# Performance work log

Hardware: AMD Instinct MI355X
Metric: run time of the kernel (lower is better)

## Reference

```python
import jax, jax.numpy as jnp
import numpy as np

N = 50000      # nodes
E = 800000     # unique directed edges (avg degree 16)
F = 64         # input_dim
D = 64         # output_dim (== F -> residual is identity)
ALPHA = 0.5
LCS_THR = 0.5  # enable_lcs_masking=True, lcs_threshold=0.5


def setup_inputs() -> dict:
    key = jax.random.key(0)
    ks = jax.random.split(key, 16)
    x = jax.random.normal(ks[0], (N, F), jnp.float32)
    src = jax.random.randint(ks[1], (E,), 0, N, jnp.int32)
    dst = jax.random.randint(ks[2], (E,), 0, N, jnp.int32)
    # integer-valued multiplicities in {1,2,3,4} (recurring-transaction counts)
    counts = jnp.floor(jax.random.uniform(ks[3], (E,), jnp.float32) * 4.0) + 1.0
    def lin(k, fan_in, shape):
        return jax.random.normal(k, shape, jnp.float32) / np.float32(np.sqrt(fan_in))
    return dict(
        x=x, counts=counts,
        W_s2d=lin(ks[4], F, (F, D)), b_s2d=jnp.zeros((D,), jnp.float32),
        W_d2s=lin(ks[5], F, (F, D)), b_d2s=jnp.zeros((D,), jnp.float32),
        W_l1=lin(ks[6], 2 * F, (2 * F, F)), b_l1=jnp.zeros((F,), jnp.float32),
        W_l2=lin(ks[7], F, (F, 1)), b_l2=jnp.zeros((1,), jnp.float32),
        W_g1=lin(ks[8], 2 * D, (2 * D, D)), b_g1=jnp.zeros((D,), jnp.float32),
        W_g2=lin(ks[9], D, (D, 1)), b_g2=jnp.zeros((1,), jnp.float32),
        src=src, dst=dst,
    )


def reference(x, counts, W_s2d, b_s2d, W_d2s, b_d2s,
              W_l1, b_l1, W_l2, b_l2, W_g1, b_g1, W_g2, b_g2,
              src, dst):
    # in/out degrees from full (unmasked) multiplicities, clamped at 1
    in_deg = jnp.maximum(jax.ops.segment_sum(counts, dst, num_segments=N), 1.0)
    out_deg = jnp.maximum(jax.ops.segment_sum(counts, src, num_segments=N), 1.0)

    # LCS per unique edge: sigmoid(MLP([x_src, x_dst])), detached in torch
    lcs_in = jnp.concatenate([x[src], x[dst]], axis=-1)          # [E, 2F]
    lcs = jax.nn.sigmoid(
        jax.nn.relu(lcs_in @ W_l1 + b_l1) @ W_l2 + b_l2)[:, 0]   # [E]
    lcs = jax.lax.stop_gradient(lcs)
    keep = (lcs >= LCS_THR).astype(x.dtype)                      # LCS masking

    # symmetric-normalized edge weights with multiplicity counts
    w = counts * keep * jax.lax.rsqrt(out_deg[src] * in_deg[dst])  # [E]

    # direction-aware message passing (redundancy-eliminated, per unique edge)
    h_s2d = x @ W_s2d + b_s2d                                    # [N, D]
    h_d2s = x @ W_d2s + b_d2s                                    # [N, D]
    m_in = jax.ops.segment_sum(w[:, None] * h_s2d[src], dst, num_segments=N)
    m_out = jax.ops.segment_sum(w[:, None] * h_d2s[dst], src, num_segments=N)

    # node-wise gating over inbound vs outbound flows
    gate = jax.nn.sigmoid(
        jax.nn.relu(jnp.concatenate([m_in, m_out], axis=-1) @ W_g1 + b_g1)
        @ W_g2 + b_g2)                                           # [N, 1]

    # gated alpha-blend + identity residual (input_dim == output_dim)
    out = ALPHA * gate * m_in + (1.0 - ALPHA) * (1.0 - gate) * m_out + x
    return out
```

## Files before the change

### kernel.cpp

```cpp
#include <hip/hip_runtime.h>
#include <math.h>


typedef unsigned long long u64;

__device__ __forceinline__ float bflo(unsigned u) { return __uint_as_float(u << 16); }
__device__ __forceinline__ float bfhi(unsigned u) { return __uint_as_float(u & 0xffff0000u); }
__device__ __forceinline__ unsigned rne16(float f) {
    unsigned u = __float_as_uint(f);
    return (u + 0x7fffu + ((u >> 16) & 1u)) >> 16;
}

__global__ void zero_kernel(int* __restrict__ p, int n) {
    int i = blockIdx.x * blockDim.x + threadIdx.x;
    int stride = gridDim.x * blockDim.x;
    for (int j = i; j < n; j += stride) p[j] = 0;
}

__global__ void finalize_deg_kernel(const u64* __restrict__ hd_pack,
                                    const u64* __restrict__ hs_pack,
                                    float* __restrict__ isq_in, float* __restrict__ isq_out, int N) {
    int i = blockIdx.x * blockDim.x + threadIdx.x;
    if (i < N) {
        isq_in[i]  = 1.f / sqrtf(fmaxf((float)(unsigned)hd_pack[i], 1.f));
        isq_out[i] = 1.f / sqrtf(fmaxf((float)(unsigned)hs_pack[i], 1.f));
    }
}

__global__ __launch_bounds__(256) void proj_kernel(
    const float* __restrict__ x,
    const float* __restrict__ Wl1,  const float* __restrict__ bl1,
    const float* __restrict__ Ws2d, const float* __restrict__ bs2d,
    const float* __restrict__ Wd2s, const float* __restrict__ bd2s,
    float* __restrict__ A, float* __restrict__ B,
    unsigned* __restrict__ Ah, unsigned* __restrict__ Bh,
    unsigned* __restrict__ HSh, unsigned* __restrict__ HDh, int N)
{
    __shared__ float xs[64][64];
    const int tid = threadIdx.x;
    const int n0  = blockIdx.x * 64;
    const int wv  = tid >> 6;
    const int cc  = tid & 63;

    const float* Wbase; const float* bias; float* obase; unsigned* obh;
    switch (wv) {
        case 0:  Wbase = Wl1;           bias = bl1;     obase = A;       obh = Ah;  break;
        case 1:  Wbase = Wl1 + 64 * 64; bias = nullptr; obase = B;       obh = Bh;  break;
        case 2:  Wbase = Ws2d;          bias = bs2d;    obase = nullptr; obh = HSh; break;
        default: Wbase = Wd2s;          bias = bd2s;    obase = nullptr; obh = HDh; break;
    }

    float wr[64];
#pragma unroll
    for (int k = 0; k < 64; ++k) wr[k] = Wbase[k * 64 + cc];
    const float bv = bias ? bias[cc] : 0.f;

#pragma unroll
    for (int j = 0; j < 4; ++j) {
        int f4  = tid + j * 256;
        int row = f4 >> 4;
        int c4  = f4 & 15;
        int gn  = n0 + row;
        float4 v = (gn < N) ? ((const float4*)x)[(long)gn * 16 + c4]
                            : make_float4(0.f, 0.f, 0.f, 0.f);
        ((float4*)&xs[row][0])[c4] = v;
    }
    __syncthreads();

    const int nmax = (N - n0 < 64) ? (N - n0) : 64;
    for (int n = 0; n < nmax; ++n) {
        float acc = bv;
#pragma unroll
        for (int k = 0; k < 64; k += 4) {
            float4 xv = *((const float4*)&xs[n][k]);
            acc += xv.x * wr[k] + xv.y * wr[k + 1] + xv.z * wr[k + 2] + xv.w * wr[k + 3];
        }
        if (obase) obase[(long)(n0 + n) * 64 + cc] = acc;
        const float part = __shfl_xor(acc, 1);
        if ((cc & 1) == 0)
            obh[(long)(n0 + n) * 32 + (cc >> 1)] = (rne16(part) << 16) | rne16(acc);
    }
}

#define LCS_MARGIN 0.04f
__global__ __launch_bounds__(256) void edge_w_kernel(
    const int* __restrict__ src, const int* __restrict__ dst,
    const float* __restrict__ counts,
    const float* __restrict__ A, const float* __restrict__ B,
    const unsigned* __restrict__ Ah, const unsigned* __restrict__ Bh,
    const float* __restrict__ Wl2, const float* __restrict__ bl2,
    unsigned char* __restrict__ keepc,
    u64* __restrict__ hd_pack, u64* __restrict__ hs_pack, int E)
{
    const int tid = threadIdx.x;
    const int e   = blockIdx.x * 16 + (tid >> 4);
    const int c   = tid & 15;
    if (e >= E) return;

    const int s = src[e];
    const int d = dst[e];
    const uint2 ua = *((const uint2*)(Ah + (long)s * 32 + c * 2));
    const uint2 ub = *((const uint2*)(Bh + (long)d * 32 + c * 2));
    const float4 wl = *((const float4*)(Wl2 + c * 4));

    float p = fmaxf(bflo(ua.x) + bflo(ub.x), 0.f) * wl.x
            + fmaxf(bfhi(ua.x) + bfhi(ub.x), 0.f) * wl.y
            + fmaxf(bflo(ua.y) + bflo(ub.y), 0.f) * wl.z
            + fmaxf(bfhi(ua.y) + bfhi(ub.y), 0.f) * wl.w;
    p += __shfl_xor(p, 1); p += __shfl_xor(p, 2);
    p += __shfl_xor(p, 4); p += __shfl_xor(p, 8);

    float z = p + bl2[0];
    if (fabsf(z) < LCS_MARGIN) {
        const float4 a = *((const float4*)(A + (long)s * 64 + c * 4));
        const float4 b = *((const float4*)(B + (long)d * 64 + c * 4));
        float q = fmaxf(a.x + b.x, 0.f) * wl.x + fmaxf(a.y + b.y, 0.f) * wl.y
                + fmaxf(a.z + b.z, 0.f) * wl.z + fmaxf(a.w + b.w, 0.f) * wl.w;
        q += __shfl_xor(q, 1); q += __shfl_xor(q, 2);
        q += __shfl_xor(q, 4); q += __shfl_xor(q, 8);
        z = q + bl2[0];
    }

    if (c == 0) {
        const u64 keep = (z >= 0.f) ? 1ull : 0ull;
        keepc[e] = (unsigned char)keep;
        const u64 ic = (u64)(unsigned)__float2int_rn(counts[e]);
        atomicAdd(hd_pack + d, (keep << 32) | ic);
        atomicAdd(hs_pack + s, (keep << 32) | ic);
    }
}

__global__ __launch_bounds__(256) void scan_reduce_kernel(
    const u64* __restrict__ hd_pack, const u64* __restrict__ hs_pack,
    int* __restrict__ bsum, int N, int NCH)
{
    __shared__ int sh[256];
    const int a = blockIdx.x / NCH;
    const int c = blockIdx.x - a * NCH;
    const u64* h = a ? hs_pack : hd_pack;
    const int idx = c * 256 + threadIdx.x;
    sh[threadIdx.x] = (idx < N) ? (int)(h[idx] >> 32) : 0;
    __syncthreads();
#pragma unroll
    for (int off = 128; off > 0; off >>= 1) {
        if (threadIdx.x < off) sh[threadIdx.x] += sh[threadIdx.x + off];
        __syncthreads();
    }
    if (threadIdx.x == 0) bsum[a * NCH + c] = sh[0];
}

__global__ __launch_bounds__(256) void scan_offsets_kernel(
    const int* __restrict__ bsum, int* __restrict__ boff, int NCH)
{
    __shared__ int sh[2][256];
    for (int a = 0; a < 2; ++a) {
        int v = (threadIdx.x < NCH) ? bsum[a * NCH + threadIdx.x] : 0;
        sh[0][threadIdx.x] = v;
        __syncthreads();
        int pb = 0;
        for (int off = 1; off < 256; off <<= 1) {
            int nv = sh[pb][threadIdx.x] + ((threadIdx.x >= off) ? sh[pb][threadIdx.x - off] : 0);
            sh[pb ^ 1][threadIdx.x] = nv;
            pb ^= 1;
            __syncthreads();
        }
        if (threadIdx.x < NCH) boff[a * NCH + threadIdx.x] = sh[pb][threadIdx.x] - v;
        __syncthreads();
    }
}

__global__ __launch_bounds__(256) void scan_write_kernel(
    const u64* __restrict__ hd_pack, const u64* __restrict__ hs_pack,
    const int* __restrict__ boff,
    int* __restrict__ rp_dst, int* __restrict__ cur_dst,
    int* __restrict__ rp_src, int* __restrict__ cur_src, int N, int NCH)
{
    __shared__ int sh[2][256];
    const int a = blockIdx.x / NCH;
    const int c = blockIdx.x - a * NCH;
    const u64* h = a ? hs_pack : hd_pack;
    int* rp  = a ? rp_src  : rp_dst;
    int* cur = a ? cur_src : cur_dst;
    const int idx = c * 256 + threadIdx.x;
    const int v = (idx < N) ? (int)(h[idx] >> 32) : 0;
    sh[0][threadIdx.x] = v;
    __syncthreads();
    int pb = 0;
    for (int off = 1; off < 256; off <<= 1) {
        int nv = sh[pb][threadIdx.x] + ((threadIdx.x >= off) ? sh[pb][threadIdx.x - off] : 0);
        sh[pb ^ 1][threadIdx.x] = nv;
        pb ^= 1;
        __syncthreads();
    }
    if (idx < N) {
        const int ex = sh[pb][threadIdx.x] - v + boff[a * NCH + c];
        rp[idx]  = ex;
        cur[idx] = ex;
    }
}

__global__ void scatter_kernel(const int* __restrict__ src, const int* __restrict__ dst,
                               const float* __restrict__ counts,
                               const unsigned char* __restrict__ keepc,
                               const float* __restrict__ isqo, const float* __restrict__ isqi,
                               int* __restrict__ cur_dst, int* __restrict__ cur_src,
                               unsigned* __restrict__ rec_dst, unsigned* __restrict__ rec_src, int E)
{
    int e = blockIdx.x * blockDim.x + threadIdx.x;
    if (e >= E) return;
    if (keepc[e]) {
        const int s = src[e];
        const int d = dst[e];
        const unsigned wb = rne16(counts[e] * isqo[s] * isqi[d]);
        int p = atomicAdd(cur_dst + d, 1);
        rec_dst[p] = ((unsigned)s << 16) | wb;
        int q = atomicAdd(cur_src + s, 1);
        rec_src[q] = ((unsigned)d << 16) | wb;
    }
}

__global__ __launch_bounds__(256) void gather_gate_kernel(
    const int* __restrict__ rp_dst, const int* __restrict__ cur_dst, const unsigned* __restrict__ rec_dst,
    const int* __restrict__ rp_src, const int* __restrict__ cur_src, const unsigned* __restrict__ rec_src,
    const unsigned* __restrict__ HSh, const unsigned* __restrict__ HDh,
    const float* __restrict__ x,
    const float* __restrict__ Wg1, const float* __restrict__ bg1,
    const float* __restrict__ Wg2, const float* __restrict__ bg2,
    float* __restrict__ out, int N)
{
    __shared__ float mbuf[4][128];
    const int tid  = threadIdx.x;
    const int wv   = tid >> 6;
    const int lane = tid & 63;
    const int g    = lane >> 3;
    const int c    = lane & 7;
    const int n    = blockIdx.x * 4 + wv;
    if (n >= N) return;

    float mi[8], mo[8];
#pragma unroll
    for (int j = 0; j < 8; ++j) { mi[j] = 0.f; mo[j] = 0.f; }

    {
        const int end = cur_dst[n];
        int i = rp_dst[n] + g;
        for (; i + 8 < end; i += 16) {
            const unsigned ra = rec_dst[i];
            const unsigned rb = rec_dst[i + 8];
            const float wa = bflo(ra), wb = bflo(rb);
            const uint4 ua = *((const uint4*)(HSh + (long)(ra >> 16) * 32 + c * 4));
            const uint4 ub = *((const uint4*)(HSh + (long)(rb >> 16) * 32 + c * 4));
            mi[0] += wa * bflo(ua.x) + wb * bflo(ub.x);
            mi[1] += wa * bfhi(ua.x) + wb * bfhi(ub.x);
            mi[2] += wa * bflo(ua.y) + wb * bflo(ub.y);
            mi[3] += wa * bfhi(ua.y) + wb * bfhi(ub.y);
            mi[4] += wa * bflo(ua.z) + wb * bflo(ub.z);
            mi[5] += wa * bfhi(ua.z) + wb * bfhi(ub.z);
            mi[6] += wa * bflo(ua.w) + wb * bflo(ub.w);
            mi[7] += wa * bfhi(ua.w) + wb * bfhi(ub.w);
        }
        if (i < end) {
            const unsigned ra = rec_dst[i];
            const float wa = bflo(ra);
            const uint4 ua = *((const uint4*)(HSh + (long)(ra >> 16) * 32 + c * 4));
            mi[0] += wa * bflo(ua.x); mi[1] += wa * bfhi(ua.x);
            mi[2] += wa * bflo(ua.y); mi[3] += wa * bfhi(ua.y);
            mi[4] += wa * bflo(ua.z); mi[5] += wa * bfhi(ua.z);
            mi[6] += wa * bflo(ua.w); mi[7] += wa * bfhi(ua.w);
        }
    }
    {
        const int end = cur_src[n];
        int i = rp_src[n] + g;
        for (; i + 8 < end; i += 16) {
            const unsigned ra = rec_src[i];
            const unsigned rb = rec_src[i + 8];
            const float wa = bflo(ra), wb = bflo(rb);
            const uint4 ua = *((const uint4*)(HDh + (long)(ra >> 16) * 32 + c * 4));
            const uint4 ub = *((const uint4*)(HDh + (long)(rb >> 16) * 32 + c * 4));
            mo[0] += wa * bflo(ua.x) + wb * bflo(ub.x);
            mo[1] += wa * bfhi(ua.x) + wb * bfhi(ub.x);
            mo[2] += wa * bflo(ua.y) + wb * bflo(ub.y);
            mo[3] += wa * bfhi(ua.y) + wb * bfhi(ub.y);
            mo[4] += wa * bflo(ua.z) + wb * bflo(ub.z);
            mo[5] += wa * bfhi(ua.z) + wb * bfhi(ub.z);
            mo[6] += wa * bflo(ua.w) + wb * bflo(ub.w);
            mo[7] += wa * bfhi(ua.w) + wb * bfhi(ub.w);
        }
        if (i < end) {
            const unsigned ra = rec_src[i];
            const float wa = bflo(ra);
            const uint4 ua = *((const uint4*)(HDh + (long)(ra >> 16) * 32 + c * 4));
            mo[0] += wa * bflo(ua.x); mo[1] += wa * bfhi(ua.x);
            mo[2] += wa * bflo(ua.y); mo[3] += wa * bfhi(ua.y);
            mo[4] += wa * bflo(ua.z); mo[5] += wa * bfhi(ua.z);
            mo[6] += wa * bflo(ua.w); mo[7] += wa * bfhi(ua.w);
        }
    }

#pragma unroll
    for (int j = 0; j < 8; ++j) {
        mi[j] += __shfl_xor(mi[j], 8);
        mi[j] += __shfl_xor(mi[j], 16);
        mi[j] += __shfl_xor(mi[j], 32);
        mo[j] += __shfl_xor(mo[j], 8);
        mo[j] += __shfl_xor(mo[j], 16);
        mo[j] += __shfl_xor(mo[j], 32);
    }
    if (g == 0) {
#pragma unroll
        for (int j = 0; j < 8; ++j) {
            mbuf[wv][c * 8 + j]      = mi[j];
            mbuf[wv][64 + c * 8 + j] = mo[j];
        }
    }

    float acc = bg1[lane];
    const float* mb = &mbuf[wv][0];
#pragma unroll 8
    for (int k4 = 0; k4 < 32; ++k4) {
        const float4 m4 = ((const float4*)mb)[k4];
        const int k = k4 * 4;
        acc += m4.x * Wg1[(k + 0) * 64 + lane] + m4.y * Wg1[(k + 1) * 64 + lane]
             + m4.z * Wg1[(k + 2) * 64 + lane] + m4.w * Wg1[(k + 3) * 64 + lane];
    }
    float v = fmaxf(acc, 0.f) * Wg2[lane];
    v += __shfl_xor(v, 1);  v += __shfl_xor(v, 2);  v += __shfl_xor(v, 4);
    v += __shfl_xor(v, 8);  v += __shfl_xor(v, 16); v += __shfl_xor(v, 32);

    const float gate = 1.f / (1.f + expf(-(v + bg2[0])));
    const float miv = mb[lane];
    const float mov = mb[64 + lane];
    out[(long)n * 64 + lane] = 0.5f * gate * miv + 0.5f * (1.f - gate) * mov
                             + x[(long)n * 64 + lane];
}

extern "C" void kernel_launch(void* const* d_in, const int* in_sizes, int n_in,
                              void* d_out, int out_size, void* d_ws, size_t ws_size,
                              hipStream_t stream) {
    const float* x      = (const float*)d_in[0];
    const float* counts = (const float*)d_in[1];
    const float* Ws2d   = (const float*)d_in[2];
    const float* bs2d   = (const float*)d_in[3];
    const float* Wd2s   = (const float*)d_in[4];
    const float* bd2s   = (const float*)d_in[5];
    const float* Wl1    = (const float*)d_in[6];
    const float* bl1    = (const float*)d_in[7];
    const float* Wl2    = (const float*)d_in[8];
    const float* bl2    = (const float*)d_in[9];
    const float* Wg1    = (const float*)d_in[10];
    const float* bg1    = (const float*)d_in[11];
    const float* Wg2    = (const float*)d_in[12];
    const float* bg2    = (const float*)d_in[13];
    const int*   src    = (const int*)d_in[14];
    const int*   dst    = (const int*)d_in[15];

    const int N   = in_sizes[0] / 64;
    const int E   = in_sizes[14];
    const int NCH = (N + 255) / 256;

    float* ws      = (float*)d_ws;
    float* isq_in  = ws;
    float* isq_out = ws + N;
    float* A       = ws + 2L * N;
    float* B       = A  + 64L * N;
    unsigned* Ah   = (unsigned*)(B + 64L * N);
    unsigned* Bh   = Ah + 32L * N;
    unsigned* HSh  = Bh + 32L * N;
    unsigned* HDh  = HSh + 32L * N;
    u64* hd_pack   = (u64*)(HDh + 32L * N);
    u64* hs_pack   = hd_pack + N;
    int* ip        = (int*)(hs_pack + N);
    int* rp_dst    = ip;
    int* cur_dst   = ip + N;
    int* rp_src    = ip + 2L * N;
    int* cur_src   = ip + 3L * N;
    int* bsum      = ip + 4L * N;
    int* boff      = bsum + 2L * NCH;
    unsigned* rec_dst = (unsigned*)(boff + 2L * NCH);
    unsigned* rec_src = rec_dst + (long)E;
    unsigned char* keepc = (unsigned char*)(rec_src + (long)E);

    zero_kernel<<<128, 256, 0, stream>>>((int*)hd_pack, 4 * N);

    proj_kernel<<<(N + 63) / 64, 256, 0, stream>>>(
        x, Wl1, bl1, Ws2d, bs2d, Wd2s, bd2s, A, B, Ah, Bh, HSh, HDh, N);

    edge_w_kernel<<<(E + 15) / 16, 256, 0, stream>>>(
        src, dst, counts, A, B, Ah, Bh, Wl2, bl2, keepc, hd_pack, hs_pack, E);

    finalize_deg_kernel<<<(N + 255) / 256, 256, 0, stream>>>(
        hd_pack, hs_pack, isq_in, isq_out, N);

    scan_reduce_kernel<<<2 * NCH, 256, 0, stream>>>(hd_pack, hs_pack, bsum, N, NCH);
    scan_offsets_kernel<<<1, 256, 0, stream>>>(bsum, boff, NCH);
    scan_write_kernel<<<2 * NCH, 256, 0, stream>>>(
        hd_pack, hs_pack, boff, rp_dst, cur_dst, rp_src, cur_src, N, NCH);

    scatter_kernel<<<(E + 255) / 256, 256, 0, stream>>>(
        src, dst, counts, keepc, isq_out , isq_in ,
        cur_dst, cur_src, rec_dst, rec_src, E);

    gather_gate_kernel<<<(N + 3) / 4, 256, 0, stream>>>(
        rp_dst, cur_dst, rec_dst, rp_src, cur_src, rec_src,
        HSh, HDh, x, Wg1, bg1, Wg2, bg2, (float*)d_out, N);
}
```

Before: 317.7 us.

## Build CSR via two-level bucket sort instead of global atomics

Replaces the global 64-bit atomic degree histogram and atomic scatter with a two-pass counting sort. A per-block coarse histogram over 256-node buckets comes first, then a local-atomic scatter, then a per-bucket fine sort that also computes degrees and row pointers. The edge kernel now writes only a bf16 weight per edge, and a patch kernel compacts kept edges into the final CSR records. This removes contended global atomics, but adds several kernels and extra passes over 2E records. It also relies on bit-packing limits such as N<65536 for the u16 node id and E<2^20 for the edge id.

```diff
diff --git a/kernel.cpp b/kernel.cpp
--- a/kernel.cpp
+++ b/kernel.cpp
@@ -3,28 +3,13 @@
 
 
 typedef unsigned long long u64;
+typedef unsigned short u16;
 
 __device__ __forceinline__ float bflo(unsigned u) { return __uint_as_float(u << 16); }
 __device__ __forceinline__ float bfhi(unsigned u) { return __uint_as_float(u & 0xffff0000u); }
 __device__ __forceinline__ unsigned rne16(float f) {
     unsigned u = __float_as_uint(f);
     return (u + 0x7fffu + ((u >> 16) & 1u)) >> 16;
-}
-
-__global__ void zero_kernel(int* __restrict__ p, int n) {
-    int i = blockIdx.x * blockDim.x + threadIdx.x;
-    int stride = gridDim.x * blockDim.x;
-    for (int j = i; j < n; j += stride) p[j] = 0;
-}
-
-__global__ void finalize_deg_kernel(const u64* __restrict__ hd_pack,
-                                    const u64* __restrict__ hs_pack,
-                                    float* __restrict__ isq_in, float* __restrict__ isq_out, int N) {
-    int i = blockIdx.x * blockDim.x + threadIdx.x;
-    if (i < N) {
-        isq_in[i]  = 1.f / sqrtf(fmaxf((float)(unsigned)hd_pack[i], 1.f));
-        isq_out[i] = 1.f / sqrtf(fmaxf((float)(unsigned)hs_pack[i], 1.f));
-    }
 }
 
 __global__ __launch_bounds__(256) void proj_kernel(
@@ -82,6 +67,173 @@
     }
 }
 
+__global__ __launch_bounds__(256) void s1_hist_kernel(
+    const int* __restrict__ src, const int* __restrict__ dst,
+    int* __restrict__ ghist, int E, int NB, int NBUCK, int chunk)
+{
+    __shared__ int hd[256], hs[256];
+    const int blk = blockIdx.x;
+    for (int i = threadIdx.x; i < NBUCK; i += 256) { hd[i] = 0; hs[i] = 0; }
+    __syncthreads();
+    const int e0 = blk * chunk;
+    const int e1 = min(E, e0 + chunk);
+    for (int e = e0 + threadIdx.x; e < e1; e += 256) {
+        atomicAdd(&hd[dst[e] >> 8], 1);
+        atomicAdd(&hs[src[e] >> 8], 1);
+    }
+    __syncthreads();
+    const int M1 = NBUCK * NB;
+    for (int b = threadIdx.x; b < NBUCK; b += 256) {
+        ghist[b * NB + blk]      = hd[b];
+        ghist[M1 + b * NB + blk] = hs[b];
+    }
+}
+
+__global__ __launch_bounds__(256) void scan_reduce_kernel(
+    const int* __restrict__ g, int* __restrict__ bsum, int M)
+{
+    __shared__ int sh[256];
+    const int idx = blockIdx.x * 256 + threadIdx.x;
+    sh[threadIdx.x] = (idx < M) ? g[idx] : 0;
+    __syncthreads();
+#pragma unroll
+    for (int off = 128; off > 0; off >>= 1) {
+        if (threadIdx.x < off) sh[threadIdx.x] += sh[threadIdx.x + off];
+        __syncthreads();
+    }
+    if (threadIdx.x == 0) bsum[blockIdx.x] = sh[0];
+}
+
+__global__ __launch_bounds__(256) void scan_offsets_kernel(
+    const int* __restrict__ bsum, int* __restrict__ boff, int NCH)
+{
+    __shared__ int sh[2][256];
+    int v = (threadIdx.x < NCH) ? bsum[threadIdx.x] : 0;
+    sh[0][threadIdx.x] = v;
+    __syncthreads();
+    int pb = 0;
+    for (int off = 1; off < 256; off <<= 1) {
+        int nv = sh[pb][threadIdx.x] + ((threadIdx.x >= off) ? sh[pb][threadIdx.x - off] : 0);
+        sh[pb ^ 1][threadIdx.x] = nv;
+        pb ^= 1;
+        __syncthreads();
+    }
+    if (threadIdx.x < NCH) boff[threadIdx.x] = sh[pb][threadIdx.x] - v;
+}
+
+__global__ __launch_bounds__(256) void scan_write_kernel(
+    const int* __restrict__ g, const int* __restrict__ boff,
+    int* __restrict__ sg, int M)
+{
+    __shared__ int sh[2][256];
+    const int idx = blockIdx.x * 256 + threadIdx.x;
+    const int v = (idx < M) ? g[idx] : 0;
+    sh[0][threadIdx.x] = v;
+    __syncthreads();
+    int pb = 0;
+    for (int off = 1; off < 256; off <<= 1) {
+        int nv = sh[pb][threadIdx.x] + ((threadIdx.x >= off) ? sh[pb][threadIdx.x - off] : 0);
+        sh[pb ^ 1][threadIdx.x] = nv;
+        pb ^= 1;
+        __syncthreads();
+    }
+    if (idx < M) sg[idx] = sh[pb][threadIdx.x] - v + boff[blockIdx.x];
+}
+
+__global__ __launch_bounds__(256) void s2_scatter_kernel(
+    const int* __restrict__ src, const int* __restrict__ dst,
+    const float* __restrict__ counts, const int* __restrict__ sghist,
+    u16* __restrict__ other, unsigned* __restrict__ eid,
+    int E, int NB, int NBUCK, int chunk)
+{
+    __shared__ int cur_d[256], cur_s[256];
+    const int blk = blockIdx.x;
+    const int M1 = NBUCK * NB;
+    for (int b = threadIdx.x; b < NBUCK; b += 256) {
+        cur_d[b] = sghist[b * NB + blk];
+        cur_s[b] = sghist[M1 + b * NB + blk];
+    }
+    __syncthreads();
+    const int e0 = blk * chunk;
+    const int e1 = min(E, e0 + chunk);
+    for (int e = e0 + threadIdx.x; e < e1; e += 256) {
+        const int s = src[e], d = dst[e];
+        const unsigned ic = (unsigned)__float2int_rn(counts[e]);
+        const unsigned meta = (unsigned)e | (ic << 20);
+        const int p = atomicAdd(&cur_d[d >> 8], 1);
+        other[p] = (u16)s;
+        eid[p]   = meta | ((unsigned)(d & 255) << 23);
+        const int q = atomicAdd(&cur_s[s >> 8], 1);
+        other[q] = (u16)d;
+        eid[q]   = meta | ((unsigned)(s & 255) << 23);
+    }
+}
+
+__global__ __launch_bounds__(256) void s3_fine_kernel(
+    const u16* __restrict__ other, const unsigned* __restrict__ eid,
+    const int* __restrict__ sghist,
+    u16* __restrict__ fother, unsigned* __restrict__ feid,
+    int* __restrict__ rpd, int* __restrict__ rps,
+    float* __restrict__ isq_in, float* __restrict__ isq_out,
+    int N, int NB, int NBUCK, int TE)
+{
+    __shared__ int cnt[256], dg[256], base[256], cur[256];
+    __shared__ int sA[256], sB[256];
+    const int tid = threadIdx.x;
+    const int dir = (blockIdx.x >= NBUCK) ? 1 : 0;
+    const int b   = blockIdx.x - dir * NBUCK;
+    const int M1  = NBUCK * NB;
+
+    const int start = sghist[dir * M1 + b * NB];
+    const int endi  = dir * M1 + (b + 1) * NB;
+    const int end   = (endi < 2 * M1) ? sghist[endi] : TE;
+
+    cnt[tid] = 0; dg[tid] = 0; cur[tid] = 0;
+    __syncthreads();
+
+    for (int i = start + tid; i < end; i += 256) {
+        const unsigned m = eid[i];
+        atomicAdd(&cnt[(m >> 23) & 255], 1);
+        atomicAdd(&dg[(m >> 23) & 255], (int)((m >> 20) & 7));
+    }
+    __syncthreads();
+
+    sA[tid] = cnt[tid];
+    __syncthreads();
+    {
+        int pb = 0;
+        int* bufs[2] = { sA, sB };
+        for (int off = 1; off < 256; off <<= 1) {
+            int nv = bufs[pb][tid] + ((tid >= off) ? bufs[pb][tid - off] : 0);
+            bufs[pb ^ 1][tid] = nv;
+            pb ^= 1;
+            __syncthreads();
+        }
+        base[tid] = bufs[pb][tid] - cnt[tid];
+    }
+    __syncthreads();
+
+    const int node = b * 256 + tid;
+    if (node < N) {
+        if (dir == 0) {
+            rpd[node]    = start + base[tid];
+            isq_in[node] = 1.f / sqrtf(fmaxf((float)dg[tid], 1.f));
+        } else {
+            rps[node]     = start + base[tid];
+            isq_out[node] = 1.f / sqrtf(fmaxf((float)dg[tid], 1.f));
+        }
+    }
+
+    for (int i = start + tid; i < end; i += 256) {
+        const unsigned m = eid[i];
+        const u16 o = other[i];
+        const int low = (m >> 23) & 255;
+        const int pos = start + base[low] + atomicAdd(&cur[low], 1);
+        fother[pos] = o;
+        feid[pos]   = m;
+    }
+}
+
 #define LCS_MARGIN 0.04f
 __global__ __launch_bounds__(256) void edge_w_kernel(
     const int* __restrict__ src, const int* __restrict__ dst,
@@ -89,8 +241,8 @@
     const float* __restrict__ A, const float* __restrict__ B,
     const unsigned* __restrict__ Ah, const unsigned* __restrict__ Bh,
     const float* __restrict__ Wl2, const float* __restrict__ bl2,
-    unsigned char* __restrict__ keepc,
-    u64* __restrict__ hd_pack, u64* __restrict__ hs_pack, int E)
+    const float* __restrict__ isqo, const float* __restrict__ isqi,
+    u16* __restrict__ wq, int E)
 {
     const int tid = threadIdx.x;
     const int e   = blockIdx.x * 16 + (tid >> 4);
@@ -122,106 +274,39 @@
     }
 
     if (c == 0) {
-        const u64 keep = (z >= 0.f) ? 1ull : 0ull;
-        keepc[e] = (unsigned char)keep;
-        const u64 ic = (u64)(unsigned)__float2int_rn(counts[e]);
-        atomicAdd(hd_pack + d, (keep << 32) | ic);
-        atomicAdd(hs_pack + s, (keep << 32) | ic);
-    }
-}
-
-__global__ __launch_bounds__(256) void scan_reduce_kernel(
-    const u64* __restrict__ hd_pack, const u64* __restrict__ hs_pack,
-    int* __restrict__ bsum, int N, int NCH)
-{
-    __shared__ int sh[256];
-    const int a = blockIdx.x / NCH;
-    const int c = blockIdx.x - a * NCH;
-    const u64* h = a ? hs_pack : hd_pack;
-    const int idx = c * 256 + threadIdx.x;
-    sh[threadIdx.x] = (idx < N) ? (int)(h[idx] >> 32) : 0;
-    __syncthreads();
-#pragma unroll
-    for (int off = 128; off > 0; off >>= 1) {
-        if (threadIdx.x < off) sh[threadIdx.x] += sh[threadIdx.x + off];
-        __syncthreads();
-    }
-    if (threadIdx.x == 0) bsum[a * NCH + c] = sh[0];
-}
-
-__global__ __launch_bounds__(256) void scan_offsets_kernel(
-    const int* __restrict__ bsum, int* __restrict__ boff, int NCH)
-{
-    __shared__ int sh[2][256];
-    for (int a = 0; a < 2; ++a) {
-        int v = (threadIdx.x < NCH) ? bsum[a * NCH + threadIdx.x] : 0;
-        sh[0][threadIdx.x] = v;
-        __syncthreads();
-        int pb = 0;
-        for (int off = 1; off < 256; off <<= 1) {
-            int nv = sh[pb][threadIdx.x] + ((threadIdx.x >= off) ? sh[pb][threadIdx.x - off] : 0);
-            sh[pb ^ 1][threadIdx.x] = nv;
-            pb ^= 1;
-            __syncthreads();
-        }
-        if (threadIdx.x < NCH) boff[a * NCH + threadIdx.x] = sh[pb][threadIdx.x] - v;
-        __syncthreads();
-    }
-}
-
-__global__ __launch_bounds__(256) void scan_write_kernel(
-    const u64* __restrict__ hd_pack, const u64* __restrict__ hs_pack,
-    const int* __restrict__ boff,
-    int* __restrict__ rp_dst, int* __restrict__ cur_dst,
-    int* __restrict__ rp_src, int* __restrict__ cur_src, int N, int NCH)
-{
-    __shared__ int sh[2][256];
-    const int a = blockIdx.x / NCH;
-    const int c = blockIdx.x - a * NCH;
-    const u64* h = a ? hs_pack : hd_pack;
-    int* rp  = a ? rp_src  : rp_dst;
-    int* cur = a ? cur_src : cur_dst;
-    const int idx = c * 256 + threadIdx.x;
-    const int v = (idx < N) ? (int)(h[idx] >> 32) : 0;
-    sh[0][threadIdx.x] = v;
-    __syncthreads();
-    int pb = 0;
-    for (int off = 1; off < 256; off <<= 1) {
-        int nv = sh[pb][threadIdx.x] + ((threadIdx.x >= off) ? sh[pb][threadIdx.x - off] : 0);
-        sh[pb ^ 1][threadIdx.x] = nv;
-        pb ^= 1;
-        __syncthreads();
-    }
-    if (idx < N) {
-        const int ex = sh[pb][threadIdx.x] - v + boff[a * NCH + c];
-        rp[idx]  = ex;
-        cur[idx] = ex;
-    }
-}
-
-__global__ void scatter_kernel(const int* __restrict__ src, const int* __restrict__ dst,
-                               const float* __restrict__ counts,
-                               const unsigned char* __restrict__ keepc,
-                               const float* __restrict__ isqo, const float* __restrict__ isqi,
-                               int* __restrict__ cur_dst, int* __restrict__ cur_src,
-                               unsigned* __restrict__ rec_dst, unsigned* __restrict__ rec_src, int E)
-{
-    int e = blockIdx.x * blockDim.x + threadIdx.x;
-    if (e >= E) return;
-    if (keepc[e]) {
-        const int s = src[e];
-        const int d = dst[e];
-        const unsigned wb = rne16(counts[e] * isqo[s] * isqi[d]);
-        int p = atomicAdd(cur_dst + d, 1);
-        rec_dst[p] = ((unsigned)s << 16) | wb;
-        int q = atomicAdd(cur_src + s, 1);
-        rec_src[q] = ((unsigned)d << 16) | wb;
-    }
+        u16 wb = 0;
+        if (z >= 0.f)
+            wb = (u16)rne16(counts[e] * isqo[s] * isqi[d]);
+        wq[e] = wb;
+    }
+}
+
+__global__ __launch_bounds__(256) void patch_kernel(
+    const u16* __restrict__ fother, const unsigned* __restrict__ feid,
+    const u16* __restrict__ wq,
+    const int* __restrict__ rpd, const int* __restrict__ rps,
+    int* __restrict__ red, int* __restrict__ res,
+    unsigned* __restrict__ rec, int N, int E)
+{
+    const int t = blockIdx.x * 256 + threadIdx.x;
+    if (t >= 2 * N) return;
+    const int dir = (t >= N) ? 1 : 0;
+    const int n   = t - dir * N;
+    const int* rp = dir ? rps : rpd;
+    const int s0  = rp[n];
+    const int s1  = (n + 1 < N) ? rp[n + 1] : (dir ? 2 * E : E);
+    int p = s0;
+    for (int i = s0; i < s1; ++i) {
+        const u16 wb = wq[feid[i] & 0xFFFFFu];
+        if (wb) rec[p++] = ((unsigned)fother[i] << 16) | (unsigned)wb;
+    }
+    (dir ? res : red)[n] = p;
 }
 
 __global__ __launch_bounds__(256) void gather_gate_kernel(
-    const int* __restrict__ rp_dst, const int* __restrict__ cur_dst, const unsigned* __restrict__ rec_dst,
-    const int* __restrict__ rp_src, const int* __restrict__ cur_src, const unsigned* __restrict__ rec_src,
+    const int* __restrict__ rpd, const int* __restrict__ red,
+    const int* __restrict__ rps, const int* __restrict__ res,
+    const unsigned* __restrict__ rec,
     const unsigned* __restrict__ HSh, const unsigned* __restrict__ HDh,
     const float* __restrict__ x,
     const float* __restrict__ Wg1, const float* __restrict__ bg1,
@@ -242,11 +327,11 @@
     for (int j = 0; j < 8; ++j) { mi[j] = 0.f; mo[j] = 0.f; }
 
     {
-        const int end = cur_dst[n];
-        int i = rp_dst[n] + g;
+        const int end = red[n];
+        int i = rpd[n] + g;
         for (; i + 8 < end; i += 16) {
-            const unsigned ra = rec_dst[i];
-            const unsigned rb = rec_dst[i + 8];
+            const unsigned ra = rec[i];
+            const unsigned rb = rec[i + 8];
             const float wa = bflo(ra), wb = bflo(rb);
             const uint4 ua = *((const uint4*)(HSh + (long)(ra >> 16) * 32 + c * 4));
             const uint4 ub = *((const uint4*)(HSh + (long)(rb >> 16) * 32 + c * 4));
@@ -260,7 +345,7 @@
             mi[7] += wa * bfhi(ua.w) + wb * bfhi(ub.w);
         }
         if (i < end) {
-            const unsigned ra = rec_dst[i];
+            const unsigned ra = rec[i];
             const float wa = bflo(ra);
             const uint4 ua = *((const uint4*)(HSh + (long)(ra >> 16) * 32 + c * 4));
             mi[0] += wa * bflo(ua.x); mi[1] += wa * bfhi(ua.x);
@@ -270,11 +355,11 @@
         }
     }
     {
-        const int end = cur_src[n];
-        int i = rp_src[n] + g;
+        const int end = res[n];
+        int i = rps[n] + g;
         for (; i + 8 < end; i += 16) {
-            const unsigned ra = rec_src[i];
-            const unsigned rb = rec_src[i + 8];
+            const unsigned ra = rec[i];
+            const unsigned rb = rec[i + 8];
             const float wa = bflo(ra), wb = bflo(rb);
             const uint4 ua = *((const uint4*)(HDh + (long)(ra >> 16) * 32 + c * 4));
             const uint4 ub = *((const uint4*)(HDh + (long)(rb >> 16) * 32 + c * 4));
@@ -288,7 +373,7 @@
             mo[7] += wa * bfhi(ua.w) + wb * bfhi(ub.w);
         }
         if (i < end) {
-            const unsigned ra = rec_src[i];
+            const unsigned ra = rec[i];
             const float wa = bflo(ra);
             const uint4 ua = *((const uint4*)(HDh + (long)(ra >> 16) * 32 + c * 4));
             mo[0] += wa * bflo(ua.x); mo[1] += wa * bfhi(ua.x);
@@ -355,53 +440,60 @@
     const int*   src    = (const int*)d_in[14];
     const int*   dst    = (const int*)d_in[15];
 
-    const int N   = in_sizes[0] / 64;
-    const int E   = in_sizes[14];
-    const int NCH = (N + 255) / 256;
-
-    float* ws      = (float*)d_ws;
-    float* isq_in  = ws;
-    float* isq_out = ws + N;
-    float* A       = ws + 2L * N;
-    float* B       = A  + 64L * N;
-    unsigned* Ah   = (unsigned*)(B + 64L * N);
-    unsigned* Bh   = Ah + 32L * N;
-    unsigned* HSh  = Bh + 32L * N;
-    unsigned* HDh  = HSh + 32L * N;
-    u64* hd_pack   = (u64*)(HDh + 32L * N);
-    u64* hs_pack   = hd_pack + N;
-    int* ip        = (int*)(hs_pack + N);
-    int* rp_dst    = ip;
-    int* cur_dst   = ip + N;
-    int* rp_src    = ip + 2L * N;
-    int* cur_src   = ip + 3L * N;
-    int* bsum      = ip + 4L * N;
-    int* boff      = bsum + 2L * NCH;
-    unsigned* rec_dst = (unsigned*)(boff + 2L * NCH);
-    unsigned* rec_src = rec_dst + (long)E;
-    unsigned char* keepc = (unsigned char*)(rec_src + (long)E);
-
-    zero_kernel<<<128, 256, 0, stream>>>((int*)hd_pack, 4 * N);
+    const int N     = in_sizes[0] / 64;
+    const int E     = in_sizes[14];
+    const int NB    = 128;
+    const int NBUCK = (N + 255) / 256;
+    const int M     = 2 * NBUCK * NB;
+    const int NCH   = (M + 255) / 256;
+    const int chunk = (E + NB - 1) / NB;
+
+    float* ws       = (float*)d_ws;
+    float* A        = ws;
+    float* B        = A + 64L * N;
+    unsigned* Ah    = (unsigned*)(B + 64L * N);
+    unsigned* Bh    = Ah + 32L * N;
+    unsigned* HSh   = Bh + 32L * N;
+    unsigned* HDh   = HSh + 32L * N;
+    float* isq_in   = (float*)(HDh + 32L * N);
+    float* isq_out  = isq_in + N;
+    int* ghist      = (int*)(isq_out + N);
+    int* sghist     = ghist + M;
+    int* bsum       = sghist + M;
+    int* boff       = bsum + NCH;
+    int* rpd        = boff + NCH;
+    int* rps        = rpd + N;
+    int* red        = rps + N;
+    int* res        = red + N;
+    u16* wq         = (u16*)(res + N);
+    u16* other      = wq + E;
+    u16* fother     = other + 2L * E;
+    unsigned* eid   = (unsigned*)(fother + 2L * E);
+    unsigned* feid  = eid + 2L * E;
+    unsigned* rec   = eid;
 
     proj_kernel<<<(N + 63) / 64, 256, 0, stream>>>(
         x, Wl1, bl1, Ws2d, bs2d, Wd2s, bd2s, A, B, Ah, Bh, HSh, HDh, N);
 
+    s1_hist_kernel<<<NB, 256, 0, stream>>>(src, dst, ghist, E, NB, NBUCK, chunk);
+    scan_reduce_kernel<<<NCH, 256, 0, stream>>>(ghist, bsum, M);
+    scan_offsets_kernel<<<1, 256, 0, stream>>>(bsum, boff, NCH);
+    scan_write_kernel<<<NCH, 256, 0, stream>>>(ghist, boff, sghist, M);
+
+    s2_scatter_kernel<<<NB, 256, 0, stream>>>(
+        src, dst, counts, sghist, other, eid, E, NB, NBUCK, chunk);
+
+    s3_fine_kernel<<<2 * NBUCK, 256, 0, stream>>>(
+        other, eid, sghist, fother, feid, rpd, rps, isq_in, isq_out,
+        N, NB, NBUCK, 2 * E);
+
     edge_w_kernel<<<(E + 15) / 16, 256, 0, stream>>>(
-        src, dst, counts, A, B, Ah, Bh, Wl2, bl2, keepc, hd_pack, hs_pack, E);
-
-    finalize_deg_kernel<<<(N + 255) / 256, 256, 0, stream>>>(
-        hd_pack, hs_pack, isq_in, isq_out, N);
-
-    scan_reduce_kernel<<<2 * NCH, 256, 0, stream>>>(hd_pack, hs_pack, bsum, N, NCH);
-    scan_offsets_kernel<<<1, 256, 0, stream>>>(bsum, boff, NCH);
-    scan_write_kernel<<<2 * NCH, 256, 0, stream>>>(
-        hd_pack, hs_pack, boff, rp_dst, cur_dst, rp_src, cur_src, N, NCH);
-
-    scatter_kernel<<<(E + 255) / 256, 256, 0, stream>>>(
-        src, dst, counts, keepc, isq_out , isq_in ,
-        cur_dst, cur_src, rec_dst, rec_src, E);
+        src, dst, counts, A, B, Ah, Bh, Wl2, bl2, isq_out, isq_in, wq, E);
+
+    patch_kernel<<<(2 * N + 255) / 256, 256, 0, stream>>>(
+        fother, feid, wq, rpd, rps, red, res, rec, N, E);
 
     gather_gate_kernel<<<(N + 3) / 4, 256, 0, stream>>>(
-        rp_dst, cur_dst, rec_dst, rp_src, cur_src, rec_src,
-        HSh, HDh, x, Wg1, bg1, Wg2, bg2, (float*)d_out, N);
-}
+        rpd, red, rps, res, rec, HSh, HDh, x, Wg1, bg1, Wg2, bg2,
+        (float*)d_out, N);
+}
```

New measurement: 340.8 us. 7.3% more time.

## Derive CSR slots from degree atomics and merge preprocessing kernels

Applied to the files above, without the earlier changes.

The edge kernel now keeps the old values returned by its packed degree atomics and stores each kept edge's slot within its dst and src buckets. That lets a new place kernel write CSR records without a second round of atomics. Zeroing is folded into the projection launch, degree inverse-sqrt is computed inside the scan-write kernel, and the two directions share one combined scan and record array. This drops four launches and a set of cursor atomics. The costs are an extra per-edge slot array, a 16-bit slot-index limit, and a scan that supports only up to 512 chunks.

```diff
diff --git a/kernel.cpp b/kernel.cpp
--- a/kernel.cpp
+++ b/kernel.cpp
@@ -3,6 +3,7 @@
 
 
 typedef unsigned long long u64;
+typedef unsigned short u16;
 
 __device__ __forceinline__ float bflo(unsigned u) { return __uint_as_float(u << 16); }
 __device__ __forceinline__ float bfhi(unsigned u) { return __uint_as_float(u & 0xffff0000u); }
@@ -11,31 +12,22 @@
     return (u + 0x7fffu + ((u >> 16) & 1u)) >> 16;
 }
 
-__global__ void zero_kernel(int* __restrict__ p, int n) {
-    int i = blockIdx.x * blockDim.x + threadIdx.x;
-    int stride = gridDim.x * blockDim.x;
-    for (int j = i; j < n; j += stride) p[j] = 0;
-}
-
-__global__ void finalize_deg_kernel(const u64* __restrict__ hd_pack,
-                                    const u64* __restrict__ hs_pack,
-                                    float* __restrict__ isq_in, float* __restrict__ isq_out, int N) {
-    int i = blockIdx.x * blockDim.x + threadIdx.x;
-    if (i < N) {
-        isq_in[i]  = 1.f / sqrtf(fmaxf((float)(unsigned)hd_pack[i], 1.f));
-        isq_out[i] = 1.f / sqrtf(fmaxf((float)(unsigned)hs_pack[i], 1.f));
-    }
-}
-
-__global__ __launch_bounds__(256) void proj_kernel(
+__global__ __launch_bounds__(256) void proj_zero_kernel(
     const float* __restrict__ x,
     const float* __restrict__ Wl1,  const float* __restrict__ bl1,
     const float* __restrict__ Ws2d, const float* __restrict__ bs2d,
     const float* __restrict__ Wd2s, const float* __restrict__ bd2s,
     float* __restrict__ A, float* __restrict__ B,
     unsigned* __restrict__ Ah, unsigned* __restrict__ Bh,
-    unsigned* __restrict__ HSh, unsigned* __restrict__ HDh, int N)
-{
+    unsigned* __restrict__ HSh, unsigned* __restrict__ HDh,
+    int* __restrict__ zp, int nzero, int PB, int N)
+{
+    if (blockIdx.x >= PB) {
+        const int t0 = (blockIdx.x - PB) * 256 + threadIdx.x;
+        const int stride = (gridDim.x - PB) * 256;
+        for (int i = t0; i < nzero; i += stride) zp[i] = 0;
+        return;
+    }
     __shared__ float xs[64][64];
     const int tid = threadIdx.x;
     const int n0  = blockIdx.x * 64;
@@ -89,8 +81,7 @@
     const float* __restrict__ A, const float* __restrict__ B,
     const unsigned* __restrict__ Ah, const unsigned* __restrict__ Bh,
     const float* __restrict__ Wl2, const float* __restrict__ bl2,
-    unsigned char* __restrict__ keepc,
-    u64* __restrict__ hd_pack, u64* __restrict__ hs_pack, int E)
+    u64* __restrict__ pk, unsigned* __restrict__ kslot, int N, int E)
 {
     const int tid = threadIdx.x;
     const int e   = blockIdx.x * 16 + (tid >> 4);
@@ -123,105 +114,100 @@
 
     if (c == 0) {
         const u64 keep = (z >= 0.f) ? 1ull : 0ull;
-        keepc[e] = (unsigned char)keep;
         const u64 ic = (u64)(unsigned)__float2int_rn(counts[e]);
-        atomicAdd(hd_pack + d, (keep << 32) | ic);
-        atomicAdd(hs_pack + s, (keep << 32) | ic);
+        const u64 od = atomicAdd(pk + d,     (keep << 32) | ic);
+        const u64 os = atomicAdd(pk + N + s, (keep << 32) | ic);
+        kslot[e] = keep ? ((((unsigned)(os >> 32)) << 16) | (unsigned)(od >> 32))
+                        : 0xFFFFFFFFu;
     }
 }
 
 __global__ __launch_bounds__(256) void scan_reduce_kernel(
-    const u64* __restrict__ hd_pack, const u64* __restrict__ hs_pack,
-    int* __restrict__ bsum, int N, int NCH)
+    const u64* __restrict__ pk, int* __restrict__ bsum, int M)
 {
     __shared__ int sh[256];
-    const int a = blockIdx.x / NCH;
-    const int c = blockIdx.x - a * NCH;
-    const u64* h = a ? hs_pack : hd_pack;
-    const int idx = c * 256 + threadIdx.x;
-    sh[threadIdx.x] = (idx < N) ? (int)(h[idx] >> 32) : 0;
+    const int idx = blockIdx.x * 256 + threadIdx.x;
+    sh[threadIdx.x] = (idx < M) ? (int)(pk[idx] >> 32) : 0;
     __syncthreads();
 #pragma unroll
     for (int off = 128; off > 0; off >>= 1) {
         if (threadIdx.x < off) sh[threadIdx.x] += sh[threadIdx.x + off];
         __syncthreads();
     }
-    if (threadIdx.x == 0) bsum[a * NCH + c] = sh[0];
-}
-
-__global__ __launch_bounds__(256) void scan_offsets_kernel(
-    const int* __restrict__ bsum, int* __restrict__ boff, int NCH)
-{
-    __shared__ int sh[2][256];
-    for (int a = 0; a < 2; ++a) {
-        int v = (threadIdx.x < NCH) ? bsum[a * NCH + threadIdx.x] : 0;
-        sh[0][threadIdx.x] = v;
+    if (threadIdx.x == 0) bsum[blockIdx.x] = sh[0];
+}
+
+__global__ __launch_bounds__(256) void scan_write_kernel(
+    const u64* __restrict__ pk, const int* __restrict__ bsum,
+    int* __restrict__ rp, int2* __restrict__ pkd, int2* __restrict__ pks,
+    int M , int N, int NCH)
+{
+    __shared__ int s0[512], s1[512];
+    const int tid = threadIdx.x;
+
+    s0[tid]       = (tid < NCH)       ? bsum[tid]       : 0;
+    s0[tid + 256] = (tid + 256 < NCH) ? bsum[tid + 256] : 0;
+    __syncthreads();
+    {
+        int* cur = s0; int* nxt = s1;
+        for (int off = 1; off < 512; off <<= 1) {
+            nxt[tid]       = cur[tid]       + ((tid >= off)       ? cur[tid - off]       : 0);
+            nxt[tid + 256] = cur[tid + 256] + ((tid + 256 >= off) ? cur[tid + 256 - off] : 0);
+            __syncthreads();
+            int* t = cur; cur = nxt; nxt = t;
+        }
+        if (tid == 0) s1[511] = 0;
         __syncthreads();
-        int pb = 0;
+        if (cur != s0) { s0[tid] = cur[tid]; s0[tid + 256] = cur[tid + 256]; __syncthreads(); }
+    }
+    const int boff = (blockIdx.x == 0) ? 0 : s0[blockIdx.x - 1];
+    __syncthreads();
+
+    const int idx = blockIdx.x * 256 + tid;
+    const u64 pv  = (idx < M) ? pk[idx] : 0ull;
+    const int v   = (int)(pv >> 32);
+    s0[tid] = v;
+    __syncthreads();
+    {
+        int* cur = s0; int* nxt = s1;
         for (int off = 1; off < 256; off <<= 1) {
-            int nv = sh[pb][threadIdx.x] + ((threadIdx.x >= off) ? sh[pb][threadIdx.x - off] : 0);
-            sh[pb ^ 1][threadIdx.x] = nv;
-            pb ^= 1;
+            nxt[tid] = cur[tid] + ((tid >= off) ? cur[tid - off] : 0);
             __syncthreads();
-        }
-        if (threadIdx.x < NCH) boff[a * NCH + threadIdx.x] = sh[pb][threadIdx.x] - v;
-        __syncthreads();
-    }
-}
-
-__global__ __launch_bounds__(256) void scan_write_kernel(
-    const u64* __restrict__ hd_pack, const u64* __restrict__ hs_pack,
-    const int* __restrict__ boff,
-    int* __restrict__ rp_dst, int* __restrict__ cur_dst,
-    int* __restrict__ rp_src, int* __restrict__ cur_src, int N, int NCH)
-{
-    __shared__ int sh[2][256];
-    const int a = blockIdx.x / NCH;
-    const int c = blockIdx.x - a * NCH;
-    const u64* h = a ? hs_pack : hd_pack;
-    int* rp  = a ? rp_src  : rp_dst;
-    int* cur = a ? cur_src : cur_dst;
-    const int idx = c * 256 + threadIdx.x;
-    const int v = (idx < N) ? (int)(h[idx] >> 32) : 0;
-    sh[0][threadIdx.x] = v;
-    __syncthreads();
-    int pb = 0;
-    for (int off = 1; off < 256; off <<= 1) {
-        int nv = sh[pb][threadIdx.x] + ((threadIdx.x >= off) ? sh[pb][threadIdx.x - off] : 0);
-        sh[pb ^ 1][threadIdx.x] = nv;
-        pb ^= 1;
-        __syncthreads();
-    }
-    if (idx < N) {
-        const int ex = sh[pb][threadIdx.x] - v + boff[a * NCH + c];
-        rp[idx]  = ex;
-        cur[idx] = ex;
-    }
-}
-
-__global__ void scatter_kernel(const int* __restrict__ src, const int* __restrict__ dst,
-                               const float* __restrict__ counts,
-                               const unsigned char* __restrict__ keepc,
-                               const float* __restrict__ isqo, const float* __restrict__ isqi,
-                               int* __restrict__ cur_dst, int* __restrict__ cur_src,
-                               unsigned* __restrict__ rec_dst, unsigned* __restrict__ rec_src, int E)
-{
-    int e = blockIdx.x * blockDim.x + threadIdx.x;
+            int* t = cur; cur = nxt; nxt = t;
+        }
+        if (idx < M) {
+            const int base = cur[tid] - v + boff;
+            rp[idx] = base;
+            const float isq = 1.f / sqrtf(fmaxf((float)(unsigned)pv, 1.f));
+            if (idx < N) pkd[idx]     = make_int2(base, __float_as_int(isq));
+            else         pks[idx - N] = make_int2(base, __float_as_int(isq));
+            if (idx == M - 1) rp[M] = base + v;
+        }
+    }
+}
+
+__global__ __launch_bounds__(256) void place_kernel(
+    const int* __restrict__ src, const int* __restrict__ dst,
+    const float* __restrict__ counts, const unsigned* __restrict__ kslot,
+    const int2* __restrict__ pkd, const int2* __restrict__ pks,
+    unsigned* __restrict__ rec, int E)
+{
+    const int e = blockIdx.x * 256 + threadIdx.x;
     if (e >= E) return;
-    if (keepc[e]) {
-        const int s = src[e];
-        const int d = dst[e];
-        const unsigned wb = rne16(counts[e] * isqo[s] * isqi[d]);
-        int p = atomicAdd(cur_dst + d, 1);
-        rec_dst[p] = ((unsigned)s << 16) | wb;
-        int q = atomicAdd(cur_src + s, 1);
-        rec_src[q] = ((unsigned)d << 16) | wb;
-    }
+    const unsigned kk = kslot[e];
+    if (kk == 0xFFFFFFFFu) return;
+    const int s = src[e];
+    const int d = dst[e];
+    const int2 qd = pkd[d];
+    const int2 qs = pks[s];
+    const float w = counts[e] * __int_as_float(qd.y) * __int_as_float(qs.y);
+    const unsigned wb = rne16(w);
+    rec[qd.x + (int)(kk & 0xFFFFu)] = ((unsigned)s << 16) | wb;
+    rec[qs.x + (int)(kk >> 16)]     = ((unsigned)d << 16) | wb;
 }
 
 __global__ __launch_bounds__(256) void gather_gate_kernel(
-    const int* __restrict__ rp_dst, const int* __restrict__ cur_dst, const unsigned* __restrict__ rec_dst,
-    const int* __restrict__ rp_src, const int* __restrict__ cur_src, const unsigned* __restrict__ rec_src,
+    const int* __restrict__ rp, const unsigned* __restrict__ rec,
     const unsigned* __restrict__ HSh, const unsigned* __restrict__ HDh,
     const float* __restrict__ x,
     const float* __restrict__ Wg1, const float* __restrict__ bg1,
@@ -242,11 +228,11 @@
     for (int j = 0; j < 8; ++j) { mi[j] = 0.f; mo[j] = 0.f; }
 
     {
-        const int end = cur_dst[n];
-        int i = rp_dst[n] + g;
+        const int end = rp[n + 1];
+        int i = rp[n] + g;
         for (; i + 8 < end; i += 16) {
-            const unsigned ra = rec_dst[i];
-            const unsigned rb = rec_dst[i + 8];
+            const unsigned ra = rec[i];
+            const unsigned rb = rec[i + 8];
             const float wa = bflo(ra), wb = bflo(rb);
             const uint4 ua = *((const uint4*)(HSh + (long)(ra >> 16) * 32 + c * 4));
             const uint4 ub = *((const uint4*)(HSh + (long)(rb >> 16) * 32 + c * 4));
@@ -260,7 +246,7 @@
             mi[7] += wa * bfhi(ua.w) + wb * bfhi(ub.w);
         }
         if (i < end) {
-            const unsigned ra = rec_dst[i];
+            const unsigned ra = rec[i];
             const float wa = bflo(ra);
             const uint4 ua = *((const uint4*)(HSh + (long)(ra >> 16) * 32 + c * 4));
             mi[0] += wa * bflo(ua.x); mi[1] += wa * bfhi(ua.x);
@@ -270,11 +256,11 @@
         }
     }
     {
-        const int end = cur_src[n];
-        int i = rp_src[n] + g;
+        const int end = rp[N + n + 1];
+        int i = rp[N + n] + g;
         for (; i + 8 < end; i += 16) {
-            const unsigned ra = rec_src[i];
-            const unsigned rb = rec_src[i + 8];
+            const unsigned ra = rec[i];
+            const unsigned rb = rec[i + 8];
             const float wa = bflo(ra), wb = bflo(rb);
             const uint4 ua = *((const uint4*)(HDh + (long)(ra >> 16) * 32 + c * 4));
             const uint4 ub = *((const uint4*)(HDh + (long)(rb >> 16) * 32 + c * 4));
@@ -288,7 +274,7 @@
             mo[7] += wa * bfhi(ua.w) + wb * bfhi(ub.w);
         }
         if (i < end) {
-            const unsigned ra = rec_src[i];
+            const unsigned ra = rec[i];
             const float wa = bflo(ra);
             const uint4 ua = *((const uint4*)(HDh + (long)(ra >> 16) * 32 + c * 4));
             mo[0] += wa * bflo(ua.x); mo[1] += wa * bfhi(ua.x);
@@ -357,51 +343,39 @@
 
     const int N   = in_sizes[0] / 64;
     const int E   = in_sizes[14];
-    const int NCH = (N + 255) / 256;
+    const int M   = 2 * N;
+    const int NCH = (M + 255) / 256;
+    const int PB  = (N + 63) / 64;
 
     float* ws      = (float*)d_ws;
-    float* isq_in  = ws;
-    float* isq_out = ws + N;
-    float* A       = ws + 2L * N;
-    float* B       = A  + 64L * N;
+    float* A       = ws;
+    float* B       = A + 64L * N;
     unsigned* Ah   = (unsigned*)(B + 64L * N);
     unsigned* Bh   = Ah + 32L * N;
     unsigned* HSh  = Bh + 32L * N;
     unsigned* HDh  = HSh + 32L * N;
-    u64* hd_pack   = (u64*)(HDh + 32L * N);
-    u64* hs_pack   = hd_pack + N;
-    int* ip        = (int*)(hs_pack + N);
-    int* rp_dst    = ip;
-    int* cur_dst   = ip + N;
-    int* rp_src    = ip + 2L * N;
-    int* cur_src   = ip + 3L * N;
-    int* bsum      = ip + 4L * N;
-    int* boff      = bsum + 2L * NCH;
-    unsigned* rec_dst = (unsigned*)(boff + 2L * NCH);
-    unsigned* rec_src = rec_dst + (long)E;
-    unsigned char* keepc = (unsigned char*)(rec_src + (long)E);
-
-    zero_kernel<<<128, 256, 0, stream>>>((int*)hd_pack, 4 * N);
-
-    proj_kernel<<<(N + 63) / 64, 256, 0, stream>>>(
-        x, Wl1, bl1, Ws2d, bs2d, Wd2s, bd2s, A, B, Ah, Bh, HSh, HDh, N);
+    u64* pk        = (u64*)(HDh + 32L * N);
+    int* bsum      = (int*)(pk + M);
+    int* rp        = bsum + 512;
+    int2* pkd      = (int2*)(rp + M + 2);
+    int2* pks      = pkd + N;
+    unsigned* kslot = (unsigned*)(pks + N);
+    unsigned* rec   = kslot + (long)E;
+
+    proj_zero_kernel<<<PB + 64, 256, 0, stream>>>(
+        x, Wl1, bl1, Ws2d, bs2d, Wd2s, bd2s, A, B, Ah, Bh, HSh, HDh,
+        (int*)pk, 4 * N, PB, N);
 
     edge_w_kernel<<<(E + 15) / 16, 256, 0, stream>>>(
-        src, dst, counts, A, B, Ah, Bh, Wl2, bl2, keepc, hd_pack, hs_pack, E);
-
-    finalize_deg_kernel<<<(N + 255) / 256, 256, 0, stream>>>(
-        hd_pack, hs_pack, isq_in, isq_out, N);
-
-    scan_reduce_kernel<<<2 * NCH, 256, 0, stream>>>(hd_pack, hs_pack, bsum, N, NCH);
-    scan_offsets_kernel<<<1, 256, 0, stream>>>(bsum, boff, NCH);
-    scan_write_kernel<<<2 * NCH, 256, 0, stream>>>(
-        hd_pack, hs_pack, boff, rp_dst, cur_dst, rp_src, cur_src, N, NCH);
-
-    scatter_kernel<<<(E + 255) / 256, 256, 0, stream>>>(
-        src, dst, counts, keepc, isq_out , isq_in ,
-        cur_dst, cur_src, rec_dst, rec_src, E);
+        src, dst, counts, A, B, Ah, Bh, Wl2, bl2, pk, kslot, N, E);
+
+    scan_reduce_kernel<<<NCH, 256, 0, stream>>>(pk, bsum, M);
+
+    scan_write_kernel<<<NCH, 256, 0, stream>>>(pk, bsum, rp, pkd, pks, M, N, NCH);
+
+    place_kernel<<<(E + 255) / 256, 256, 0, stream>>>(
+        src, dst, counts, kslot, pkd, pks, rec, E);
 
     gather_gate_kernel<<<(N + 3) / 4, 256, 0, stream>>>(
-        rp_dst, cur_dst, rec_dst, rp_src, cur_src, rec_src,
-        HSh, HDh, x, Wg1, bg1, Wg2, bg2, (float*)d_out, N);
-}
+        rp, rec, HSh, HDh, x, Wg1, bg1, Wg2, bg2, (float*)d_out, N);
+}
```

Result: faster. 293.4 us (-7.6%).
